# Performance work log

Measured on AMD Instinct MI355X. Metric: run time of the kernel, lower is better.

Reference implementation:

```python
import jax, jax.numpy as jnp
import numpy as np

N = 400000
CIN = 32
COUT = 64
K = 27  # 3x3x3 kernel offsets
EPS = 1e-5


def setup_inputs() -> dict:
    key = jax.random.key(0)
    ks = jax.random.split(key, 16)
    feats = jax.random.normal(ks[0], (N, CIN), dtype=jnp.float32)
    # neighbor tables: one neighbor per kernel offset; center offset = self
    def nbrs(k):
        n = jax.random.randint(k, (N, K), 0, N, dtype=jnp.int32)
        return n.at[:, K // 2].set(jnp.arange(N, dtype=jnp.int32))
    nbr1 = nbrs(ks[1])
    nbr3 = nbrs(ks[2])
    nbr9 = nbrs(ks[3])
    s = lambda cin: 1.0 / np.sqrt(cin * K)
    W0a = jax.random.normal(ks[4], (K, CIN, COUT), dtype=jnp.float32) * s(CIN)
    W0b = jax.random.normal(ks[5], (K, COUT, COUT), dtype=jnp.float32) * s(COUT)
    g1 = jnp.ones((COUT,), jnp.float32)
    b1 = jnp.zeros((COUT,), jnp.float32)
    g2 = jnp.ones((COUT,), jnp.float32)
    b2 = jnp.zeros((COUT,), jnp.float32)
    Wlin = jax.random.normal(ks[6], (CIN, COUT), dtype=jnp.float32) / np.sqrt(CIN)
    Wsw = jax.random.normal(ks[7], (COUT, 3 * COUT), dtype=jnp.float32) / np.sqrt(COUT)
    scale0 = jnp.ones((COUT,), jnp.float32)          # Scale(out, 1.0)
    scale1 = jnp.full((COUT,), 0.01, jnp.float32)    # Scale(out, 0.01)
    return {"feats": feats, "nbr1": nbr1, "nbr3": nbr3, "nbr9": nbr9,
            "W0a": W0a, "g1": g1, "b1": b1, "W0b": W0b, "g2": g2, "b2": b2,
            "Wlin": Wlin, "Wsw": Wsw, "scale0": scale0, "scale1": scale1}


def sparse_conv(f, nbr, W):
    # gather-matmul-accumulate over the K kernel offsets
    out = jnp.zeros((f.shape[0], W.shape[-1]), f.dtype)
    for k in range(W.shape[0]):
        out = out + jnp.take(f, nbr[:, k], axis=0) @ W[k]
    return out


def batchnorm(f, g, b):
    mu = jnp.mean(f, axis=0)
    var = jnp.var(f, axis=0)
    return (f - mu) * jax.lax.rsqrt(var + EPS) * g + b


def pool(f, nbr):
    # average over the kernel neighborhood
    acc = jnp.zeros_like(f)
    for k in range(nbr.shape[1]):
        acc = acc + jnp.take(f, nbr[:, k], axis=0)
    return acc / nbr.shape[1]


def reference(feats, nbr1, nbr3, nbr9, W0a, g1, b1, W0b, g2, b2, Wlin, Wsw, scale0, scale1):
    # conv0: two ConvBlocks (sparse conv -> BN -> ReLU)
    x0 = jax.nn.relu(batchnorm(sparse_conv(feats, nbr1, W0a), g1, b1))
    x0 = jax.nn.relu(batchnorm(sparse_conv(x0, nbr1, W0b), g2, b2))
    # residual through 1x1 lin (in_channels != out_channels)
    x0 = x0 + feats @ Wlin
    # multi-scale pooling chain (dilation 1, 3, 9)
    x1 = pool(x0, nbr1)
    x2 = pool(x1, nbr3)
    x3 = pool(x2, nbr9)
    # switch: 1x1 conv -> [N,3,C] gates, weighted sum of the three scales
    gates = (x0 @ Wsw).reshape(x0.shape[0], 3, COUT)
    f2 = x1 * gates[:, 0] + x2 * gates[:, 1] + x3 * gates[:, 2]
    # y = scale0*x0 + dropout(scale1*f2); dropout in eval mode (identity)
    return scale0 * x0 + scale1 * f2
```

## Files before the change

kernel.cpp:

```cpp
#include <hip/hip_runtime.h>

#define CIN  32
#define COUT 64
#define KK   27
#define EPSV 1e-5f

__device__ __forceinline__ float bf_lo(unsigned u) { return __uint_as_float(u << 16); }
__device__ __forceinline__ float bf_hi(unsigned u) { return __uint_as_float(u & 0xffff0000u); }
__device__ __forceinline__ unsigned f2bf(float x) {
    unsigned u = __float_as_uint(x);
    return (u + 0x7fffu + ((u >> 16) & 1u)) >> 16;
}
__device__ __forceinline__ unsigned pack2(float a, float b) { return f2bf(a) | (f2bf(b) << 16); }

__global__ __launch_bounds__(256) void k_conv1(
    const float* __restrict__ feats, const int* __restrict__ nbr,
    const float* __restrict__ W, float* __restrict__ t1, unsigned* __restrict__ t1h, int n)
{
    int half = __builtin_amdgcn_readfirstlane(threadIdx.x >> 7);
    int cbase = half * 32;
    int p  = blockIdx.x * 128 + (threadIdx.x & 127);
    int pc = p < n ? p : n - 1;
    float acc[32];
#pragma unroll
    for (int c = 0; c < 32; c++) acc[c] = 0.f;
    const int* np = nbr + (size_t)pc * KK;

#pragma unroll 1
    for (int k = 0; k < KK; k++) {
        int idx = np[k];
        const float4* fr = (const float4*)(feats + (size_t)idx * CIN);
        float4 b[8];
#pragma unroll
        for (int q = 0; q < 8; q++) b[q] = fr[q];
        const float* Wk = W + k * (CIN * COUT) + cbase;
#pragma unroll 2
        for (int q = 0; q < 8; q++) {
            float fv[4] = {b[q].x, b[q].y, b[q].z, b[q].w};
#pragma unroll
            for (int e = 0; e < 4; e++) {
                float fj = fv[e];
                const float* wr = Wk + (q * 4 + e) * COUT;
#pragma unroll
                for (int c = 0; c < 32; c++) acc[c] = fmaf(fj, wr[c], acc[c]);
            }
        }
    }
    if (p < n) {
        float4* o = (float4*)(t1 + (size_t)p * COUT + cbase);
#pragma unroll
        for (int q = 0; q < 8; q++)
            o[q] = make_float4(acc[4*q], acc[4*q+1], acc[4*q+2], acc[4*q+3]);
        uint4* oh = (uint4*)(t1h + (size_t)p * (COUT / 2) + half * 16);
#pragma unroll
        for (int q = 0; q < 4; q++) {
            uint4 h;
            h.x = pack2(acc[8*q+0], acc[8*q+1]);
            h.y = pack2(acc[8*q+2], acc[8*q+3]);
            h.z = pack2(acc[8*q+4], acc[8*q+5]);
            h.w = pack2(acc[8*q+6], acc[8*q+7]);
            oh[q] = h;
        }
    }
}

__global__ __launch_bounds__(256) void k_sum(const float* __restrict__ x, int n,
                                             float* __restrict__ S)
{
    __shared__ float ls[2 * COUT];
    if (threadIdx.x < 2 * COUT) ls[threadIdx.x] = 0.f;
    __syncthreads();
    long long total4 = (long long)n * (COUT / 4);
    long long stride = (long long)gridDim.x * 256;
    float s0 = 0, s1 = 0, s2 = 0, s3 = 0, q0 = 0, q1 = 0, q2 = 0, q3 = 0;
    for (long long i = (long long)blockIdx.x * 256 + threadIdx.x; i < total4; i += stride) {
        float4 v = ((const float4*)x)[i];
        s0 += v.x; q0 += v.x * v.x;
        s1 += v.y; q1 += v.y * v.y;
        s2 += v.z; q2 += v.z * v.z;
        s3 += v.w; q3 += v.w * v.w;
    }
    int cb = (threadIdx.x * 4) & (COUT - 1);
    atomicAdd(&ls[cb + 0], s0); atomicAdd(&ls[cb + 1], s1);
    atomicAdd(&ls[cb + 2], s2); atomicAdd(&ls[cb + 3], s3);
    atomicAdd(&ls[COUT + cb + 0], q0); atomicAdd(&ls[COUT + cb + 1], q1);
    atomicAdd(&ls[COUT + cb + 2], q2); atomicAdd(&ls[COUT + cb + 3], q3);
    __syncthreads();
    if (threadIdx.x < 2 * COUT) atomicAdd(&S[threadIdx.x], ls[threadIdx.x]);
}

__global__ __launch_bounds__(256) void k_conv2(
    const unsigned* __restrict__ t1h, const int* __restrict__ nbr,
    const float* __restrict__ W, const float* __restrict__ S,
    const float* __restrict__ g, const float* __restrict__ b,
    float* __restrict__ t2, int n, float invn)
{
    __shared__ float sA[COUT], sB[COUT];
    if (threadIdx.x < COUT) {
        int c = threadIdx.x;
        float mu  = S[c] * invn;
        float var = fmaxf(S[COUT + c] * invn - mu * mu, 0.f);
        float a   = g[c] * rsqrtf(var + EPSV);
        sA[c] = a; sB[c] = b[c] - mu * a;
    }
    __syncthreads();
    int half = __builtin_amdgcn_readfirstlane(threadIdx.x >> 7);
    int cbase = half * 32;
    int p  = blockIdx.x * 128 + (threadIdx.x & 127);
    int pc = p < n ? p : n - 1;
    float acc[32];
#pragma unroll
    for (int c = 0; c < 32; c++) acc[c] = 0.f;
    const int* np = nbr + (size_t)pc * KK;

#pragma unroll 1
    for (int k = 0; k < KK; k++) {
        int idx = np[k];
        const uint4* fr = (const uint4*)(t1h + (size_t)idx * (COUT / 2));
        uint4 bv[8];
#pragma unroll
        for (int q = 0; q < 8; q++) bv[q] = fr[q];
        const float* Wk = W + k * (COUT * COUT) + cbase;
#pragma unroll 1
        for (int jc = 0; jc < 4; jc++) {
            float f[16];
#pragma unroll
            for (int h = 0; h < 2; h++) {
                uint4 v = bv[jc * 2 + h];
                f[h*8+0] = bf_lo(v.x); f[h*8+1] = bf_hi(v.x);
                f[h*8+2] = bf_lo(v.y); f[h*8+3] = bf_hi(v.y);
                f[h*8+4] = bf_lo(v.z); f[h*8+5] = bf_hi(v.z);
                f[h*8+6] = bf_lo(v.w); f[h*8+7] = bf_hi(v.w);
            }
#pragma unroll
            for (int jj = 0; jj < 16; jj++) {
                int j = jc * 16 + jj;
                f[jj] = fmaxf(fmaf(f[jj], sA[j], sB[j]), 0.f);
            }
#pragma unroll 4
            for (int jj = 0; jj < 16; jj++) {
                float fj = f[jj];
                const float* wr = Wk + (jc * 16 + jj) * COUT;
#pragma unroll
                for (int c = 0; c < 32; c++) acc[c] = fmaf(fj, wr[c], acc[c]);
            }
        }
    }
    if (p < n) {
        float4* o = (float4*)(t2 + (size_t)p * COUT + cbase);
#pragma unroll
        for (int q = 0; q < 8; q++)
            o[q] = make_float4(acc[4*q], acc[4*q+1], acc[4*q+2], acc[4*q+3]);
    }
}

__global__ __launch_bounds__(256) void k_x0(
    const float* t2, const float* __restrict__ feats,
    const float* __restrict__ S, const float* __restrict__ g, const float* __restrict__ b,
    const float* __restrict__ Wlin, float* x0f, unsigned* __restrict__ x0h,
    int n, float invn)
{
    __shared__ float sA[COUT], sB[COUT];
    if (threadIdx.x < COUT) {
        int c = threadIdx.x;
        float mu  = S[c] * invn;
        float var = fmaxf(S[COUT + c] * invn - mu * mu, 0.f);
        float a   = g[c] * rsqrtf(var + EPSV);
        sA[c] = a; sB[c] = b[c] - mu * a;
    }
    __syncthreads();
    int p  = blockIdx.x * 256 + threadIdx.x;
    int pc = p < n ? p : n - 1;
    float f[CIN];
    {
        const float4* fr = (const float4*)(feats + (size_t)pc * CIN);
#pragma unroll
        for (int q = 0; q < CIN / 4; q++) {
            float4 v = fr[q];
            f[4*q+0] = v.x; f[4*q+1] = v.y; f[4*q+2] = v.z; f[4*q+3] = v.w;
        }
    }
    float acc[COUT];
    {
        const float4* tr = (const float4*)(t2 + (size_t)pc * COUT);
#pragma unroll
        for (int q = 0; q < COUT / 4; q++) {
            float4 v = tr[q];
            acc[4*q+0] = fmaxf(fmaf(v.x, sA[4*q+0], sB[4*q+0]), 0.f);
            acc[4*q+1] = fmaxf(fmaf(v.y, sA[4*q+1], sB[4*q+1]), 0.f);
            acc[4*q+2] = fmaxf(fmaf(v.z, sA[4*q+2], sB[4*q+2]), 0.f);
            acc[4*q+3] = fmaxf(fmaf(v.w, sA[4*q+3], sB[4*q+3]), 0.f);
        }
    }
#pragma unroll 4
    for (int j = 0; j < CIN; j++) {
        float fj = f[j];
        const float* wr = Wlin + j * COUT;
#pragma unroll
        for (int c = 0; c < COUT; c++) acc[c] = fmaf(fj, wr[c], acc[c]);
    }
    if (p < n) {
        float4* o = (float4*)(x0f + (size_t)p * COUT);
#pragma unroll
        for (int q = 0; q < COUT / 4; q++)
            o[q] = make_float4(acc[4*q], acc[4*q+1], acc[4*q+2], acc[4*q+3]);
        uint4* oh = (uint4*)(x0h + (size_t)p * (COUT / 2));
#pragma unroll
        for (int q = 0; q < COUT / 8; q++) {
            uint4 h;
            h.x = pack2(acc[8*q+0], acc[8*q+1]);
            h.y = pack2(acc[8*q+2], acc[8*q+3]);
            h.z = pack2(acc[8*q+4], acc[8*q+5]);
            h.w = pack2(acc[8*q+6], acc[8*q+7]);
            oh[q] = h;
        }
    }
}

__global__ __launch_bounds__(256) void k_pool(
    const unsigned* __restrict__ x, const int* __restrict__ nbr,
    unsigned* __restrict__ y, int n)
{
    int gt = blockIdx.x * 256 + threadIdx.x;
    int p  = gt >> 1;
    int half = gt & 1;
    int pc = p < n ? p : n - 1;
    float acc[32];
#pragma unroll
    for (int c = 0; c < 32; c++) acc[c] = 0.f;
    const int* np = nbr + (size_t)pc * KK;

#pragma unroll 1
    for (int k = 0; k < KK; k++) {
        int idx = np[k];
        const uint4* r = (const uint4*)(x + (size_t)idx * (COUT / 2) + half * 16);
        uint4 bv[4];
#pragma unroll
        for (int q = 0; q < 4; q++) bv[q] = r[q];
#pragma unroll
        for (int q = 0; q < 4; q++) {
            uint4 v = bv[q];
            acc[q*8+0] += bf_lo(v.x); acc[q*8+1] += bf_hi(v.x);
            acc[q*8+2] += bf_lo(v.y); acc[q*8+3] += bf_hi(v.y);
            acc[q*8+4] += bf_lo(v.z); acc[q*8+5] += bf_hi(v.z);
            acc[q*8+6] += bf_lo(v.w); acc[q*8+7] += bf_hi(v.w);
        }
    }
    if (p < n) {
        const float inv = 1.f / 27.f;
        uint4* o = (uint4*)(y + (size_t)p * (COUT / 2) + half * 16);
#pragma unroll
        for (int q = 0; q < 4; q++) {
            uint4 h;
            h.x = pack2(acc[8*q+0]*inv, acc[8*q+1]*inv);
            h.y = pack2(acc[8*q+2]*inv, acc[8*q+3]*inv);
            h.z = pack2(acc[8*q+4]*inv, acc[8*q+5]*inv);
            h.w = pack2(acc[8*q+6]*inv, acc[8*q+7]*inv);
            o[q] = h;
        }
    }
}

__global__ __launch_bounds__(192) void k_final2(
    const float* __restrict__ x0f, const unsigned* __restrict__ x1h,
    const unsigned* __restrict__ x2h, const unsigned* __restrict__ x3h,
    const float* __restrict__ Wsw, const float* __restrict__ sc0,
    const float* __restrict__ sc1, float* __restrict__ out, int n)
{
    __shared__ float xs[192 * 65];
    int p  = blockIdx.x * 192 + threadIdx.x;
    int pc = p < n ? p : n - 1;
    float* myx = xs + threadIdx.x * 65;
    {
        const float4* xr = (const float4*)(x0f + (size_t)pc * COUT);
#pragma unroll
        for (int q = 0; q < COUT / 4; q++) {
            float4 v = xr[q];
            myx[4*q+0] = v.x; myx[4*q+1] = v.y; myx[4*q+2] = v.z; myx[4*q+3] = v.w;
        }
    }

#pragma unroll 1
    for (int ch = 0; ch < 4; ch++) {
        int cb = ch * 16;
        float g0[16], g1[16], g2[16];
#pragma unroll
        for (int i = 0; i < 16; i++) { g0[i] = 0.f; g1[i] = 0.f; g2[i] = 0.f; }
#pragma unroll 2
        for (int j = 0; j < COUT; j++) {
            float fj = myx[j];
            const float* wr = Wsw + j * 192 + cb;
#pragma unroll
            for (int cc = 0; cc < 16; cc++) {
                g0[cc] = fmaf(fj, wr[cc],        g0[cc]);
                g1[cc] = fmaf(fj, wr[64 + cc],   g1[cc]);
                g2[cc] = fmaf(fj, wr[128 + cc],  g2[cc]);
            }
        }
        if (p < n) {
            const uint4* r1 = (const uint4*)(x1h + (size_t)pc * (COUT/2) + cb/2);
            const uint4* r2 = (const uint4*)(x2h + (size_t)pc * (COUT/2) + cb/2);
            const uint4* r3 = (const uint4*)(x3h + (size_t)pc * (COUT/2) + cb/2);
            uint4 a0 = r1[0], a1 = r1[1];
            uint4 b0 = r2[0], b1 = r2[1];
            uint4 c0 = r3[0], c1 = r3[1];
            float x1v[16], x2v[16], x3v[16];
            x1v[0]=bf_lo(a0.x); x1v[1]=bf_hi(a0.x); x1v[2]=bf_lo(a0.y); x1v[3]=bf_hi(a0.y);
            x1v[4]=bf_lo(a0.z); x1v[5]=bf_hi(a0.z); x1v[6]=bf_lo(a0.w); x1v[7]=bf_hi(a0.w);
            x1v[8]=bf_lo(a1.x); x1v[9]=bf_hi(a1.x); x1v[10]=bf_lo(a1.y); x1v[11]=bf_hi(a1.y);
            x1v[12]=bf_lo(a1.z); x1v[13]=bf_hi(a1.z); x1v[14]=bf_lo(a1.w); x1v[15]=bf_hi(a1.w);
            x2v[0]=bf_lo(b0.x); x2v[1]=bf_hi(b0.x); x2v[2]=bf_lo(b0.y); x2v[3]=bf_hi(b0.y);
            x2v[4]=bf_lo(b0.z); x2v[5]=bf_hi(b0.z); x2v[6]=bf_lo(b0.w); x2v[7]=bf_hi(b0.w);
            x2v[8]=bf_lo(b1.x); x2v[9]=bf_hi(b1.x); x2v[10]=bf_lo(b1.y); x2v[11]=bf_hi(b1.y);
            x2v[12]=bf_lo(b1.z); x2v[13]=bf_hi(b1.z); x2v[14]=bf_lo(b1.w); x2v[15]=bf_hi(b1.w);
            x3v[0]=bf_lo(c0.x); x3v[1]=bf_hi(c0.x); x3v[2]=bf_lo(c0.y); x3v[3]=bf_hi(c0.y);
            x3v[4]=bf_lo(c0.z); x3v[5]=bf_hi(c0.z); x3v[6]=bf_lo(c0.w); x3v[7]=bf_hi(c0.w);
            x3v[8]=bf_lo(c1.x); x3v[9]=bf_hi(c1.x); x3v[10]=bf_lo(c1.y); x3v[11]=bf_hi(c1.y);
            x3v[12]=bf_lo(c1.z); x3v[13]=bf_hi(c1.z); x3v[14]=bf_lo(c1.w); x3v[15]=bf_hi(c1.w);
            float ov[16];
#pragma unroll
            for (int cc = 0; cc < 16; cc++) {
                float f2 = x1v[cc] * g0[cc] + x2v[cc] * g1[cc] + x3v[cc] * g2[cc];
                ov[cc] = sc0[cb + cc] * myx[cb + cc] + sc1[cb + cc] * f2;
            }
            float4* o = (float4*)(out + (size_t)p * COUT + cb);
#pragma unroll
            for (int q = 0; q < 4; q++)
                o[q] = make_float4(ov[4*q], ov[4*q+1], ov[4*q+2], ov[4*q+3]);
        }
    }
}

extern "C" void kernel_launch(void* const* d_in, const int* in_sizes, int n_in,
                              void* d_out, int out_size, void* d_ws, size_t ws_size,
                              hipStream_t stream)
{
    const float* feats = (const float*)d_in[0];
    const int*   nbr1  = (const int*)d_in[1];
    const int*   nbr3  = (const int*)d_in[2];
    const int*   nbr9  = (const int*)d_in[3];
    const float* W0a   = (const float*)d_in[4];
    const float* g1    = (const float*)d_in[5];
    const float* b1    = (const float*)d_in[6];
    const float* W0b   = (const float*)d_in[7];
    const float* g2    = (const float*)d_in[8];
    const float* b2    = (const float*)d_in[9];
    const float* Wlin  = (const float*)d_in[10];
    const float* Wsw   = (const float*)d_in[11];
    const float* sc0   = (const float*)d_in[12];
    const float* sc1   = (const float*)d_in[13];

    int n = in_sizes[0] / CIN;
    float* base = (float*)d_ws;
    float*    A   = base;
    unsigned* t1h = (unsigned*)(base + (size_t)n * COUT);
    unsigned* x0h = t1h + (size_t)n * (COUT / 2);
    unsigned* x1h = x0h + (size_t)n * (COUT / 2);
    unsigned* x2h = x1h + (size_t)n * (COUT / 2);
    unsigned* x3h = x2h + (size_t)n * (COUT / 2);
    float*    S   = (float*)(x3h + (size_t)n * (COUT / 2));
    float*    out = (float*)d_out;
    float invn = 1.0f / (float)n;

    int gridH = (n + 127) / 128;
    int grid  = (n + 255) / 256;
    int gridF = (n + 191) / 192;

    hipMemsetAsync(S, 0, 256 * sizeof(float), stream);
    k_conv1<<<gridH, 256, 0, stream>>>(feats, nbr1, W0a, A, t1h, n);
    k_sum<<<2048, 256, 0, stream>>>(A, n, S);
    k_conv2<<<gridH, 256, 0, stream>>>(t1h, nbr1, W0b, S, g1, b1, A, n, invn);
    k_sum<<<2048, 256, 0, stream>>>(A, n, S + 128);
    k_x0<<<grid, 256, 0, stream>>>(A, feats, S + 128, g2, b2, Wlin, A, x0h, n, invn);
    k_pool<<<gridH, 256, 0, stream>>>(x0h, nbr1, x1h, n);
    k_pool<<<gridH, 256, 0, stream>>>(x1h, nbr3, x2h, n);
    k_pool<<<gridH, 256, 0, stream>>>(x2h, nbr9, x3h, n);
    k_final2<<<gridF, 192, 0, stream>>>(A, x1h, x2h, x3h, Wsw, sc0, sc1, out, n);
}
```

Baseline: 4.570 ms.

## Split conv reduction dimension across thread halves and combine partials via LDS

Both sparse-conv kernels now split the input-channel (reduction) dimension between the two 128-thread halves of a block instead of the output channels. Each thread gathers only half of each neighbor row and accumulates all 64 outputs, and the partial sums are then exchanged through shared memory. This halves the per-thread gather traffic, so the two halves no longer load the same full row. The cost is 64 accumulators per thread, which raises register pressure, plus an LDS reduction with three barriers. Launch bounds are also set to request 4 blocks per CU.

```diff
diff --git a/kernel.cpp b/kernel.cpp
--- a/kernel.cpp
+++ b/kernel.cpp
@@ -13,53 +13,94 @@
 }
 __device__ __forceinline__ unsigned pack2(float a, float b) { return f2bf(a) | (f2bf(b) << 16); }
 
-__global__ __launch_bounds__(256) void k_conv1(
+__global__ __launch_bounds__(256, 4) void k_conv1(
     const float* __restrict__ feats, const int* __restrict__ nbr,
     const float* __restrict__ W, float* __restrict__ t1, unsigned* __restrict__ t1h, int n)
 {
+    __shared__ float comb[128][33];
     int half = __builtin_amdgcn_readfirstlane(threadIdx.x >> 7);
-    int cbase = half * 32;
-    int p  = blockIdx.x * 128 + (threadIdx.x & 127);
+    int jbase = half * 16;
+    int lp = threadIdx.x & 127;
+    int p  = blockIdx.x * 128 + lp;
     int pc = p < n ? p : n - 1;
-    float acc[32];
-#pragma unroll
-    for (int c = 0; c < 32; c++) acc[c] = 0.f;
+    float accA[32], accB[32];
+#pragma unroll
+    for (int c = 0; c < 32; c++) { accA[c] = 0.f; accB[c] = 0.f; }
     const int* np = nbr + (size_t)pc * KK;
 
 #pragma unroll 1
     for (int k = 0; k < KK; k++) {
         int idx = np[k];
-        const float4* fr = (const float4*)(feats + (size_t)idx * CIN);
-        float4 b[8];
-#pragma unroll
-        for (int q = 0; q < 8; q++) b[q] = fr[q];
-        const float* Wk = W + k * (CIN * COUT) + cbase;
-#pragma unroll 2
-        for (int q = 0; q < 8; q++) {
+        const float4* fr = (const float4*)(feats + (size_t)idx * CIN + jbase);
+        float4 b[4];
+#pragma unroll
+        for (int q = 0; q < 4; q++) b[q] = fr[q];
+        const float* Wk = W + k * (CIN * COUT);
+#pragma unroll
+        for (int q = 0; q < 4; q++) {
             float fv[4] = {b[q].x, b[q].y, b[q].z, b[q].w};
 #pragma unroll
             for (int e = 0; e < 4; e++) {
                 float fj = fv[e];
-                const float* wr = Wk + (q * 4 + e) * COUT;
-#pragma unroll
-                for (int c = 0; c < 32; c++) acc[c] = fmaf(fj, wr[c], acc[c]);
-            }
-        }
+                const float* wr = Wk + (jbase + q * 4 + e) * COUT;
+#pragma unroll
+                for (int c = 0; c < 32; c++) {
+                    accA[c] = fmaf(fj, wr[c],      accA[c]);
+                    accB[c] = fmaf(fj, wr[32 + c], accB[c]);
+                }
+            }
+        }
+    }
+    if (half == 0) {
+#pragma unroll
+        for (int i = 0; i < 32; i++) comb[lp][i] = accB[i];
+    }
+    __syncthreads();
+    if (half == 1) {
+#pragma unroll
+        for (int i = 0; i < 32; i++) accB[i] += comb[lp][i];
+    }
+    __syncthreads();
+    if (half == 1) {
+#pragma unroll
+        for (int i = 0; i < 32; i++) comb[lp][i] = accA[i];
+    }
+    __syncthreads();
+    if (half == 0) {
+#pragma unroll
+        for (int i = 0; i < 32; i++) accA[i] += comb[lp][i];
     }
     if (p < n) {
-        float4* o = (float4*)(t1 + (size_t)p * COUT + cbase);
-#pragma unroll
-        for (int q = 0; q < 8; q++)
-            o[q] = make_float4(acc[4*q], acc[4*q+1], acc[4*q+2], acc[4*q+3]);
-        uint4* oh = (uint4*)(t1h + (size_t)p * (COUT / 2) + half * 16);
-#pragma unroll
-        for (int q = 0; q < 4; q++) {
-            uint4 h;
-            h.x = pack2(acc[8*q+0], acc[8*q+1]);
-            h.y = pack2(acc[8*q+2], acc[8*q+3]);
-            h.z = pack2(acc[8*q+4], acc[8*q+5]);
-            h.w = pack2(acc[8*q+6], acc[8*q+7]);
-            oh[q] = h;
+        if (half == 0) {
+            float4* o = (float4*)(t1 + (size_t)p * COUT);
+#pragma unroll
+            for (int q = 0; q < 8; q++)
+                o[q] = make_float4(accA[4*q], accA[4*q+1], accA[4*q+2], accA[4*q+3]);
+            uint4* oh = (uint4*)(t1h + (size_t)p * (COUT / 2));
+#pragma unroll
+            for (int q = 0; q < 4; q++) {
+                uint4 h;
+                h.x = pack2(accA[8*q+0], accA[8*q+1]);
+                h.y = pack2(accA[8*q+2], accA[8*q+3]);
+                h.z = pack2(accA[8*q+4], accA[8*q+5]);
+                h.w = pack2(accA[8*q+6], accA[8*q+7]);
+                oh[q] = h;
+            }
+        } else {
+            float4* o = (float4*)(t1 + (size_t)p * COUT + 32);
+#pragma unroll
+            for (int q = 0; q < 8; q++)
+                o[q] = make_float4(accB[4*q], accB[4*q+1], accB[4*q+2], accB[4*q+3]);
+            uint4* oh = (uint4*)(t1h + (size_t)p * (COUT / 2) + 16);
+#pragma unroll
+            for (int q = 0; q < 4; q++) {
+                uint4 h;
+                h.x = pack2(accB[8*q+0], accB[8*q+1]);
+                h.y = pack2(accB[8*q+2], accB[8*q+3]);
+                h.z = pack2(accB[8*q+4], accB[8*q+5]);
+                h.w = pack2(accB[8*q+6], accB[8*q+7]);
+                oh[q] = h;
+            }
         }
     }
 }
@@ -89,13 +130,14 @@
     if (threadIdx.x < 2 * COUT) atomicAdd(&S[threadIdx.x], ls[threadIdx.x]);
 }
 
-__global__ __launch_bounds__(256) void k_conv2(
+__global__ __launch_bounds__(256, 4) void k_conv2(
     const unsigned* __restrict__ t1h, const int* __restrict__ nbr,
     const float* __restrict__ W, const float* __restrict__ S,
     const float* __restrict__ g, const float* __restrict__ b,
     float* __restrict__ t2, int n, float invn)
 {
     __shared__ float sA[COUT], sB[COUT];
+    __shared__ float comb[128][33];
     if (threadIdx.x < COUT) {
         int c = threadIdx.x;
         float mu  = S[c] * invn;
@@ -105,52 +147,79 @@
     }
     __syncthreads();
     int half = __builtin_amdgcn_readfirstlane(threadIdx.x >> 7);
-    int cbase = half * 32;
-    int p  = blockIdx.x * 128 + (threadIdx.x & 127);
+    int jbase = half * 32;
+    int lp = threadIdx.x & 127;
+    int p  = blockIdx.x * 128 + lp;
     int pc = p < n ? p : n - 1;
-    float acc[32];
-#pragma unroll
-    for (int c = 0; c < 32; c++) acc[c] = 0.f;
+    float accA[32], accB[32];
+#pragma unroll
+    for (int c = 0; c < 32; c++) { accA[c] = 0.f; accB[c] = 0.f; }
     const int* np = nbr + (size_t)pc * KK;
 
 #pragma unroll 1
     for (int k = 0; k < KK; k++) {
         int idx = np[k];
-        const uint4* fr = (const uint4*)(t1h + (size_t)idx * (COUT / 2));
-        uint4 bv[8];
-#pragma unroll
-        for (int q = 0; q < 8; q++) bv[q] = fr[q];
-        const float* Wk = W + k * (COUT * COUT) + cbase;
-#pragma unroll 1
-        for (int jc = 0; jc < 4; jc++) {
-            float f[16];
-#pragma unroll
-            for (int h = 0; h < 2; h++) {
-                uint4 v = bv[jc * 2 + h];
-                f[h*8+0] = bf_lo(v.x); f[h*8+1] = bf_hi(v.x);
-                f[h*8+2] = bf_lo(v.y); f[h*8+3] = bf_hi(v.y);
-                f[h*8+4] = bf_lo(v.z); f[h*8+5] = bf_hi(v.z);
-                f[h*8+6] = bf_lo(v.w); f[h*8+7] = bf_hi(v.w);
-            }
-#pragma unroll
-            for (int jj = 0; jj < 16; jj++) {
-                int j = jc * 16 + jj;
-                f[jj] = fmaxf(fmaf(f[jj], sA[j], sB[j]), 0.f);
-            }
-#pragma unroll 4
-            for (int jj = 0; jj < 16; jj++) {
-                float fj = f[jj];
-                const float* wr = Wk + (jc * 16 + jj) * COUT;
-#pragma unroll
-                for (int c = 0; c < 32; c++) acc[c] = fmaf(fj, wr[c], acc[c]);
-            }
-        }
+        const uint4* fr = (const uint4*)(t1h + (size_t)idx * (COUT / 2) + half * 16);
+        uint4 bv[4];
+#pragma unroll
+        for (int q = 0; q < 4; q++) bv[q] = fr[q];
+        const float* Wk = W + k * (COUT * COUT);
+#pragma unroll
+        for (int q = 0; q < 4; q++) {
+            uint4 v = bv[q];
+            float f[8];
+            f[0] = bf_lo(v.x); f[1] = bf_hi(v.x);
+            f[2] = bf_lo(v.y); f[3] = bf_hi(v.y);
+            f[4] = bf_lo(v.z); f[5] = bf_hi(v.z);
+            f[6] = bf_lo(v.w); f[7] = bf_hi(v.w);
+#pragma unroll
+            for (int i = 0; i < 8; i++) {
+                int j = jbase + q * 8 + i;
+                f[i] = fmaxf(fmaf(f[i], sA[j], sB[j]), 0.f);
+            }
+#pragma unroll
+            for (int i = 0; i < 8; i++) {
+                float fj = f[i];
+                const float* wr = Wk + (jbase + q * 8 + i) * COUT;
+#pragma unroll
+                for (int c = 0; c < 32; c++) {
+                    accA[c] = fmaf(fj, wr[c],      accA[c]);
+                    accB[c] = fmaf(fj, wr[32 + c], accB[c]);
+                }
+            }
+        }
+    }
+    if (half == 0) {
+#pragma unroll
+        for (int i = 0; i < 32; i++) comb[lp][i] = accB[i];
+    }
+    __syncthreads();
+    if (half == 1) {
+#pragma unroll
+        for (int i = 0; i < 32; i++) accB[i] += comb[lp][i];
+    }
+    __syncthreads();
+    if (half == 1) {
+#pragma unroll
+        for (int i = 0; i < 32; i++) comb[lp][i] = accA[i];
+    }
+    __syncthreads();
+    if (half == 0) {
+#pragma unroll
+        for (int i = 0; i < 32; i++) accA[i] += comb[lp][i];
     }
     if (p < n) {
-        float4* o = (float4*)(t2 + (size_t)p * COUT + cbase);
-#pragma unroll
-        for (int q = 0; q < 8; q++)
-            o[q] = make_float4(acc[4*q], acc[4*q+1], acc[4*q+2], acc[4*q+3]);
+        if (half == 0) {
+            float4* o = (float4*)(t2 + (size_t)p * COUT);
+#pragma unroll
+            for (int q = 0; q < 8; q++)
+                o[q] = make_float4(accA[4*q], accA[4*q+1], accA[4*q+2], accA[4*q+3]);
+        } else {
+            float4* o = (float4*)(t2 + (size_t)p * COUT + 32);
+#pragma unroll
+            for (int q = 0; q < 8; q++)
+                o[q] = make_float4(accB[4*q], accB[4*q+1], accB[4*q+2], accB[4*q+3]);
+        }
     }
 }
 
```

Result: slower. 5.225 ms (+14.3%).
